# Performance work log

Hardware: AMD Instinct MI355X
Metric: run time of the kernel (lower is better)

## Reference

```python
import jax, jax.numpy as jnp
import numpy as np

EPS = 1e-6
LAMB = 0.1
ITERS = 3


def setup_inputs() -> dict:
    key = jax.random.key(0)
    k = jax.random.split(key, 6)
    bi, bt, R, W, D = 128, 128, 36, 50, 1024
    return {
        "img_cls": jax.random.normal(k[0], (bi, D), jnp.float32),
        "imgs": jax.random.normal(k[1], (bi, R, D), jnp.float32),
        "cap_cls": jax.random.normal(k[2], (bt, D), jnp.float32),
        "caps": jax.random.normal(k[3], (bt, W, D), jnp.float32),
        "img_lens": jax.random.randint(k[4], (bi,), 1, R + 1, jnp.int32),
        "cap_lens": jax.random.randint(k[5], (bt,), 1, W + 1, jnp.int32),
    }


def _bregman(cost, mask, r, c):
    # P = exp(-cost/lamb) (masked entries have cost=+inf -> P=0), then
    # iterative row/col rescaling toward marginals r, c.
    P = jnp.where(mask, jnp.exp(-cost / LAMB), 0.0)
    P = P / (jnp.sum(P, axis=(-2, -1), keepdims=True) + EPS)
    for _ in range(ITERS):
        u = P.sum(axis=-1) + EPS          # [bi,bt,R]
        P = P * (r / u)[..., None]
        v = P.sum(axis=-2) + EPS          # [bi,bt,W]
        P = P * (c / v)[:, :, None, :]
    return P


def reference(img_cls, imgs, cap_cls, caps, img_lens, cap_lens):
    imgs = imgs + EPS
    caps = caps + EPS
    # prepend cls token
    imgs = jnp.concatenate([img_cls[:, None, :], imgs], axis=1)   # [bi,R+1,D]
    caps = jnp.concatenate([cap_cls[:, None, :], caps], axis=1)   # [bt,W+1,D]
    imgs = imgs / jnp.linalg.norm(imgs, axis=-1, keepdims=True)
    caps = caps / jnp.linalg.norm(caps, axis=-1, keepdims=True)
    # fine-grained cosine sims: [bi, bt, R+1, W+1]
    fg_sims = jnp.einsum("ird,twd->itrw", imgs, caps)
    il = img_lens + 1
    cl = cap_lens + 1
    R1, W1 = imgs.shape[1], caps.shape[1]
    rmask = jnp.arange(R1)[None, :] < il[:, None]   # [bi,R+1]
    wmask = jnp.arange(W1)[None, :] < cl[:, None]   # [bt,W+1]
    mask = rmask[:, None, :, None] & wmask[None, :, None, :]  # [bi,bt,R+1,W+1]
    # _ave_init: uniform marginals over valid rows/cols
    rvalid = mask.any(axis=-1).astype(fg_sims.dtype)  # [bi,bt,R+1]
    cvalid = mask.any(axis=-2).astype(fg_sims.dtype)  # [bi,bt,W+1]
    r = rvalid / rvalid.sum(axis=-1, keepdims=True)
    c = cvalid / cvalid.sum(axis=-1, keepdims=True)
    cost = 1.0 - fg_sims
    tp = _bregman(cost, mask, r, c)
    sims = jnp.sum(fg_sims * tp * mask.astype(fg_sims.dtype), axis=(-2, -1))
    return sims  # [bi, bt]
```

## Files before the change

### kernel.cpp

```cpp
#include <hip/hip_runtime.h>
#include <hip/hip_fp16.h>

#define EPSF 1e-6f

typedef _Float16 f16x8 __attribute__((ext_vector_type(8)));
typedef float f32x4 __attribute__((ext_vector_type(4)));

#define BK 32
#define SMEM_BYTES 49152
#define BUF_BYTES 18432

#define AS1 __attribute__((address_space(1)))
#define AS3 __attribute__((address_space(3)))

#define VM_WAIT(N) asm volatile("s_waitcnt vmcnt(" #N ")" ::: "memory")
#define LGKM0()    asm volatile("s_waitcnt lgkmcnt(0)" ::: "memory")

template <int CTRL>
__device__ __forceinline__ float dpp_add(float x) {
    int y = __builtin_amdgcn_update_dpp(0, __float_as_int(x), CTRL, 0xf, 0xf, true);
    return x + __int_as_float(y);
}

__device__ __forceinline__ float wave_sum_bc(float x) {
    x = dpp_add<0xB1>(x);
    x = dpp_add<0x4E>(x);
    x = dpp_add<0x141>(x);
    x = dpp_add<0x140>(x);
    x = dpp_add<0x142>(x);
    x = dpp_add<0x143>(x);
    return __int_as_float(__builtin_amdgcn_readlane(__float_as_int(x), 63));
}

__global__ __launch_bounds__(256) void norm_kernel(
        const float* __restrict__ img_cls, const float* __restrict__ imgs,
        const float* __restrict__ cap_cls, const float* __restrict__ caps,
        __half* __restrict__ Ah, __half* __restrict__ Bh) {
    __shared__ float red[4];
    const int row = blockIdx.x;
    const int tid = threadIdx.x;

    const float* src = nullptr;
    __half* dst;
    float eps_add = EPSF;
    if (row < 64 * 80) {
        const int g = row / 80, r = row % 80;
        dst = Ah + (size_t)row * 1024;
        int i = -1, rr = 0;
        if (r < 37)      { i = 2 * g;     rr = r; }
        else if (r < 74) { i = 2 * g + 1; rr = r - 37; }
        if (i >= 0) {
            if (rr == 0) { src = img_cls + (size_t)i * 1024; eps_add = 0.0f; }
            else         { src = imgs + ((size_t)i * 36 + (rr - 1)) * 1024; }
        }
    } else {
        const int row2 = row - 64 * 80;
        const int t = row2 >> 6, r = row2 & 63;
        dst = Bh + (size_t)row2 * 1024;
        if (r == 0)       { src = cap_cls + (size_t)t * 1024; eps_add = 0.0f; }
        else if (r <= 50) { src = caps + ((size_t)t * 50 + (r - 1)) * 1024; }
    }

    if (src == nullptr) {
        ushort4 z; z.x = z.y = z.z = z.w = 0;
        reinterpret_cast<ushort4*>(dst)[tid] = z;
        return;
    }

    float4 v = reinterpret_cast<const float4*>(src)[tid];
    v.x += eps_add; v.y += eps_add; v.z += eps_add; v.w += eps_add;
    float ss = v.x * v.x + v.y * v.y + v.z * v.z + v.w * v.w;
    #pragma unroll
    for (int m = 1; m <= 32; m <<= 1) ss += __shfl_xor(ss, m);
    if ((tid & 63) == 0) red[tid >> 6] = ss;
    __syncthreads();
    const float tot = red[0] + red[1] + red[2] + red[3];
    const float rn = 1.0f / sqrtf(tot);

    ushort4 o;
    o.x = __half_as_ushort(__float2half(v.x * rn));
    o.y = __half_as_ushort(__float2half(v.y * rn));
    o.z = __half_as_ushort(__float2half(v.z * rn));
    o.w = __half_as_ushort(__float2half(v.w * rn));
    reinterpret_cast<ushort4*>(dst)[tid] = o;
}

__device__ __forceinline__ void stage_oct(const __half* __restrict__ Ag,
                                          const __half* __restrict__ Bg,
                                          __half* buf, int kb, int o, size_t lofs) {
    const __half* src = (o < 10) ? (Ag + (size_t)o * 16384 + kb + lofs)
                                 : (Bg + (size_t)(o - 10) * 16384 + kb + lofs);
    __builtin_amdgcn_global_load_lds((const AS1 void*)src,
                                     (AS3 void*)(buf + o * 512), 16, 0, 0);
}

__device__ __forceinline__ void stage_tile(const __half* __restrict__ Ag,
                                           const __half* __restrict__ Bg,
                                           __half* buf, int kb, int wave,
                                           size_t lofs) {
    stage_oct(Ag, Bg, buf, kb, wave, lofs);
    stage_oct(Ag, Bg, buf, kb, wave + 4, lofs);
    stage_oct(Ag, Bg, buf, kb, wave + 8, lofs);
    stage_oct(Ag, Bg, buf, kb, wave + 12, lofs);
    if (wave < 2) stage_oct(Ag, Bg, buf, kb, wave + 16, lofs);
}

__device__ __forceinline__ void ds_loads32(const __half* buf, int wm, int wn,
                                           int fr, int q4, f16x8 af[5], f16x8 bf[4]) {
    const int soff = ((q4 ^ ((fr >> 1) & 3)) * 8);
    #pragma unroll
    for (int n = 0; n < 4; ++n) {
        const int R = 160 + wn * 64 + n * 16 + fr;
        bf[n] = *reinterpret_cast<const f16x8*>(buf + R * BK + soff);
    }
    #pragma unroll
    for (int m = 0; m < 5; ++m) {
        const int R = wm * 80 + m * 16 + fr;
        af[m] = *reinterpret_cast<const f16x8*>(buf + R * BK + soff);
    }
}

__device__ __forceinline__ void mfma_cluster(f32x4 acc[5][4], const f16x8 af[5],
                                             const f16x8 bf[4]) {
    __builtin_amdgcn_s_setprio(1);
    #pragma unroll
    for (int m = 0; m < 5; ++m)
        #pragma unroll
        for (int n = 0; n < 4; ++n)
            acc[m][n] = __builtin_amdgcn_mfma_f32_16x16x32_f16(af[m], bf[n], acc[m][n], 0, 0, 0);
    __builtin_amdgcn_s_setprio(0);
}

__global__ __launch_bounds__(256, 3) void fused_kernel(
        const __half* __restrict__ Ah, const __half* __restrict__ Bh,
        const int* __restrict__ img_lens, const int* __restrict__ cap_lens,
        float* __restrict__ out) {
    __shared__ __align__(16) char smem[SMEM_BYTES];
    __half* lds0 = reinterpret_cast<__half*>(smem);
    __half* lds1 = reinterpret_cast<__half*>(smem + BUF_BYTES);

    const int idx = blockIdx.x;
    const int xcd = idx & 7;
    const int within = idx >> 3;
    const int bx = within >> 3;
    const int by = xcd * 8 + (within & 7);

    const int tid = threadIdx.x;
    const int wave = tid >> 6;
    const int lane = tid & 63;
    const int wm = wave >> 1, wn = wave & 1;
    const int fr = lane & 15;
    const int q4 = lane >> 4;

    const __half* Ag = Ah + (size_t)bx * 160 * 1024;
    const __half* Bg = Bh + (size_t)by * 2 * 64 * 1024;

    const int rsub = lane >> 2;
    const int segsrc = (lane & 3) ^ ((lane >> 3) & 3);
    const size_t lofs = (size_t)rsub * 1024 + (size_t)(segsrc * 8);

    f32x4 acc[5][4];
    #pragma unroll
    for (int m = 0; m < 5; ++m)
        #pragma unroll
        for (int n = 0; n < 4; ++n) {
            f32x4 z = {0.0f, 0.0f, 0.0f, 0.0f};
            acc[m][n] = z;
        }

    stage_tile(Ag, Bg, lds0, 0, wave, lofs);
    stage_tile(Ag, Bg, lds1, BK, wave, lofs);
    if (wave < 2) { VM_WAIT(5); } else { VM_WAIT(4); }
    __builtin_amdgcn_s_barrier();

    #pragma unroll 2
    for (int kt = 0; kt < 30; ++kt) {
        __half* cur = (kt & 1) ? lds1 : lds0;
        f16x8 af[5], bf[4];
        ds_loads32(cur, wm, wn, fr, q4, af, bf);
        mfma_cluster(acc, af, bf);
        LGKM0();
        __builtin_amdgcn_s_barrier();
        stage_tile(Ag, Bg, cur, (kt + 2) * BK, wave, lofs);
        if (wave < 2) { VM_WAIT(5); } else { VM_WAIT(4); }
        __builtin_amdgcn_s_barrier();
    }
    {
        f16x8 af[5], bf[4];
        ds_loads32(lds0, wm, wn, fr, q4, af, bf);
        mfma_cluster(acc, af, bf);
        VM_WAIT(0);
        __builtin_amdgcn_s_barrier();
    }
    {
        f16x8 af[5], bf[4];
        ds_loads32(lds1, wm, wn, fr, q4, af, bf);
        mfma_cluster(acc, af, bf);
    }

    __syncthreads();

    float* fg = reinterpret_cast<float*>(smem) + wave * (48 * 64);
    const int orow = q4 * 4;

    #pragma unroll
    for (int p = 0; p < 2; ++p) {
        if (p) {
            LGKM0();
        }
        #pragma unroll
        for (int pm = 0; pm < 3; ++pm) {
            #pragma unroll
            for (int n = 0; n < 4; ++n) {
                const int colbase = (n * 16 + fr) ^ (q4 << 4);
                #pragma unroll
                for (int q = 0; q < 4; ++q)
                    fg[(pm * 16 + orow + q) * 64 + colbase] = acc[pm + 2 * p][n][q];
            }
        }

        const int i = 4 * bx + 2 * wm + p;
        const int t = 2 * by + wn;
        const int il = img_lens[i] + 1;
        const int cl = cap_lens[t] + 1;
        const bool vcol = lane < cl;
        const int rbase = p ? 5 : 0;

        #define FGR(r_) fg[((r_) + rbase) * 64 + \
                           (lane ^ (((((r_) + rbase) >> 2) & 3) << 4))]

        float P[37];
        float ts[4] = {0.f, 0.f, 0.f, 0.f};
        #pragma unroll
        for (int r = 0; r < 37; ++r) {
            if (r < il) {
                const float f = FGR(r);
                const float pe = vcol ? __expf((f - 1.0f) * 10.0f) : 0.0f;
                P[r] = pe;
                ts[r & 3] += pe;
            } else {
                P[r] = 0.0f;
            }
        }
        float tot = (ts[0] + ts[1]) + (ts[2] + ts[3]);
        tot = wave_sum_bc(tot);
        const float s0 = __builtin_amdgcn_rcpf(tot + EPSF);
        #pragma unroll
        for (int r = 0; r < 37; ++r) P[r] *= s0;

        const float rmarg = 1.0f / (float)il;
        const float cmarg = 1.0f / (float)cl;
        for (int it = 0; it < 3; ++it) {
            #pragma unroll
            for (int r = 0; r < 37; ++r) {
                if (r < il) {
                    const float u = wave_sum_bc(P[r]);
                    P[r] *= rmarg * __builtin_amdgcn_rcpf(u + EPSF);
                }
            }
            float vs[4] = {EPSF, 0.f, 0.f, 0.f};
            #pragma unroll
            for (int r = 0; r < 37; ++r) vs[r & 3] += P[r];
            const float v = (vs[0] + vs[1]) + (vs[2] + vs[3]);
            const float cs = vcol ? cmarg * __builtin_amdgcn_rcpf(v) : 0.0f;
            #pragma unroll
            for (int r = 0; r < 37; ++r) P[r] *= cs;
        }

        float ls[4] = {0.f, 0.f, 0.f, 0.f};
        #pragma unroll
        for (int r = 0; r < 37; ++r) {
            if (r < il) ls[r & 3] += FGR(r) * P[r];
        }
        float local = (ls[0] + ls[1]) + (ls[2] + ls[3]);
        local = wave_sum_bc(local);
        if (lane == 0) out[i * 128 + t] = local;
        #undef FGR
    }
}

extern "C" void kernel_launch(void* const* d_in, const int* in_sizes, int n_in,
                              void* d_out, int out_size, void* d_ws, size_t ws_size,
                              hipStream_t stream) {
    const float* img_cls  = (const float*)d_in[0];
    const float* imgs     = (const float*)d_in[1];
    const float* cap_cls  = (const float*)d_in[2];
    const float* caps     = (const float*)d_in[3];
    const int*   img_lens = (const int*)d_in[4];
    const int*   cap_lens = (const int*)d_in[5];
    float* out = (float*)d_out;

    __half* Ah = (__half*)d_ws;
    __half* Bh = Ah + (size_t)64 * 80 * 1024;

    norm_kernel<<<64 * 80 + 128 * 64, 256, 0, stream>>>(img_cls, imgs, cap_cls, caps, Ah, Bh);
    fused_kernel<<<2048, 256, 0, stream>>>(Ah, Bh, img_lens, cap_lens, out);
}
```

Measured before the change: 159.7 us.

## Load B fragments directly from global into registers, stage only A in LDS

The GEMM main loop no longer stages the B (caption) tile through LDS. Each wave now loads its B fragments straight from global memory into registers, double-buffered one k-step ahead, while A still goes through async global-to-LDS double buffering. This shrinks the LDS buffer and the ds_read traffic per step, but adds uncoalesced-ish per-wave global loads of B that are duplicated across the waves sharing the same wn, and more complex vmcnt accounting.

```diff
diff --git a/kernel.cpp b/kernel.cpp
--- a/kernel.cpp
+++ b/kernel.cpp
@@ -8,7 +8,7 @@
 
 #define BK 32
 #define SMEM_BYTES 49152
-#define BUF_BYTES 18432
+#define BUF_BYTES 10240
 
 #define AS1 __attribute__((address_space(1)))
 #define AS3 __attribute__((address_space(3)))
@@ -85,39 +85,36 @@
     reinterpret_cast<ushort4*>(dst)[tid] = o;
 }
 
-__device__ __forceinline__ void stage_oct(const __half* __restrict__ Ag,
-                                          const __half* __restrict__ Bg,
-                                          __half* buf, int kb, int o, size_t lofs) {
-    const __half* src = (o < 10) ? (Ag + (size_t)o * 16384 + kb + lofs)
-                                 : (Bg + (size_t)(o - 10) * 16384 + kb + lofs);
+__device__ __forceinline__ void stage_octA(const __half* __restrict__ Ag,
+                                           __half* buf, int kb, int o, size_t lofs) {
+    const __half* src = Ag + (size_t)o * 16384 + kb + lofs;
     __builtin_amdgcn_global_load_lds((const AS1 void*)src,
                                      (AS3 void*)(buf + o * 512), 16, 0, 0);
 }
 
-__device__ __forceinline__ void stage_tile(const __half* __restrict__ Ag,
-                                           const __half* __restrict__ Bg,
-                                           __half* buf, int kb, int wave,
-                                           size_t lofs) {
-    stage_oct(Ag, Bg, buf, kb, wave, lofs);
-    stage_oct(Ag, Bg, buf, kb, wave + 4, lofs);
-    stage_oct(Ag, Bg, buf, kb, wave + 8, lofs);
-    stage_oct(Ag, Bg, buf, kb, wave + 12, lofs);
-    if (wave < 2) stage_oct(Ag, Bg, buf, kb, wave + 16, lofs);
-}
-
-__device__ __forceinline__ void ds_loads32(const __half* buf, int wm, int wn,
-                                           int fr, int q4, f16x8 af[5], f16x8 bf[4]) {
+__device__ __forceinline__ void stage_A(const __half* __restrict__ Ag,
+                                        __half* buf, int kb, int wave, size_t lofs) {
+    stage_octA(Ag, buf, kb, wave, lofs);
+    stage_octA(Ag, buf, kb, wave + 4, lofs);
+    if (wave < 2) stage_octA(Ag, buf, kb, wave + 8, lofs);
+}
+
+__device__ __forceinline__ void ds_af(const __half* buf, int wm, int fr, int q4,
+                                      f16x8 af[5]) {
     const int soff = ((q4 ^ ((fr >> 1) & 3)) * 8);
-    #pragma unroll
-    for (int n = 0; n < 4; ++n) {
-        const int R = 160 + wn * 64 + n * 16 + fr;
-        bf[n] = *reinterpret_cast<const f16x8*>(buf + R * BK + soff);
-    }
     #pragma unroll
     for (int m = 0; m < 5; ++m) {
         const int R = wm * 80 + m * 16 + fr;
         af[m] = *reinterpret_cast<const f16x8*>(buf + R * BK + soff);
     }
+}
+
+__device__ __forceinline__ void load_bf(const __half* __restrict__ Bg, int kt,
+                                        int wn, int fr, int q4, f16x8 bf[4]) {
+    const __half* p = Bg + (size_t)(wn * 64 + fr) * 1024 + q4 * 8 + kt * BK;
+    #pragma unroll
+    for (int n = 0; n < 4; ++n)
+        bf[n] = *reinterpret_cast<const f16x8*>(p + (size_t)n * 16 * 1024);
 }
 
 __device__ __forceinline__ void mfma_cluster(f32x4 acc[5][4], const f16x8 af[5],
@@ -168,34 +165,50 @@
             acc[m][n] = z;
         }
 
-    stage_tile(Ag, Bg, lds0, 0, wave, lofs);
-    stage_tile(Ag, Bg, lds1, BK, wave, lofs);
-    if (wave < 2) { VM_WAIT(5); } else { VM_WAIT(4); }
+    f16x8 bfA[4], bfB[4];
+
+    load_bf(Bg, 0, wn, fr, q4, bfA);
+    stage_A(Ag, lds0, 0, wave, lofs);
+    stage_A(Ag, lds1, BK, wave, lofs);
+    if (wave < 2) { VM_WAIT(3); } else { VM_WAIT(2); }
     __builtin_amdgcn_s_barrier();
 
-    #pragma unroll 2
-    for (int kt = 0; kt < 30; ++kt) {
-        __half* cur = (kt & 1) ? lds1 : lds0;
-        f16x8 af[5], bf[4];
-        ds_loads32(cur, wm, wn, fr, q4, af, bf);
-        mfma_cluster(acc, af, bf);
+    #define GEMM_TILE(KT, LDSBUF, CUR, NXT)                               \
+    {                                                                     \
+        f16x8 af[5];                                                      \
+        ds_af((LDSBUF), wm, fr, q4, af);                                  \
+        if (wave < 2) { VM_WAIT(3); } else { VM_WAIT(2); }                \
+        load_bf(Bg, (KT) + 1, wn, fr, q4, (NXT));                         \
+        mfma_cluster(acc, af, (CUR));                                     \
+        LGKM0();                                                          \
+        __builtin_amdgcn_s_barrier();                                     \
+        stage_A(Ag, (LDSBUF), ((KT) + 2) * BK, wave, lofs);               \
+        if (wave < 2) { VM_WAIT(7); } else { VM_WAIT(6); }                \
+        __builtin_amdgcn_s_barrier();                                     \
+    }
+
+    #pragma unroll 1
+    for (int kt = 0; kt < 30; kt += 2) {
+        GEMM_TILE(kt, lds0, bfA, bfB);
+        GEMM_TILE(kt + 1, lds1, bfB, bfA);
+    }
+    #undef GEMM_TILE
+
+    {
+        f16x8 af[5];
+        ds_af(lds0, wm, fr, q4, af);
+        if (wave < 2) { VM_WAIT(3); } else { VM_WAIT(2); }
+        load_bf(Bg, 31, wn, fr, q4, bfB);
+        mfma_cluster(acc, af, bfA);
         LGKM0();
+        VM_WAIT(4);
         __builtin_amdgcn_s_barrier();
-        stage_tile(Ag, Bg, cur, (kt + 2) * BK, wave, lofs);
-        if (wave < 2) { VM_WAIT(5); } else { VM_WAIT(4); }
-        __builtin_amdgcn_s_barrier();
     }
     {
-        f16x8 af[5], bf[4];
-        ds_loads32(lds0, wm, wn, fr, q4, af, bf);
-        mfma_cluster(acc, af, bf);
+        f16x8 af[5];
+        ds_af(lds1, wm, fr, q4, af);
         VM_WAIT(0);
-        __builtin_amdgcn_s_barrier();
-    }
-    {
-        f16x8 af[5], bf[4];
-        ds_loads32(lds1, wm, wn, fr, q4, af, bf);
-        mfma_cluster(acc, af, bf);
+        mfma_cluster(acc, af, bfB);
     }
 
     __syncthreads();
```

Result: slower. 205.9 us (+28.9%).
